# Kernel optimization log

Hardware: AMD Instinct MI355X
Metric: run time of the kernel (lower is better)

## Reference

```python
import jax, jax.numpy as jnp
import numpy as np

S, N, F_IN, F_OUT = 8, 4096, 128, 128


def setup_inputs() -> dict:
    key = jax.random.key(0)
    ks = jax.random.split(key, 7)
    return {
        "theta": jax.random.normal(ks[0], (S,), dtype=jnp.float32),
        "T_slices": jax.random.normal(ks[1], (S, N, N), dtype=jnp.float32),
        "x": jax.random.normal(ks[2], (N, F_IN), dtype=jnp.float32),
        "a": jax.random.uniform(ks[3], (N, N), dtype=jnp.float32),
        "W_fc": jax.random.normal(ks[4], (F_OUT, F_IN), dtype=jnp.float32) * (1.0 / np.sqrt(F_IN)),
        "b_fc": jax.random.normal(ks[5], (F_OUT,), dtype=jnp.float32) * 0.01,
        "prelu_alpha": jnp.full((F_IN,), 0.25, dtype=jnp.float32),
    }


def reference(theta, T_slices, x, a, W_fc, b_fc, prelu_alpha):
    # q = sum_s theta[s] * T_slices[s]  -> [N, N]
    q = jnp.einsum("s,snm->nm", theta, T_slices)
    # mask by adjacency (the torch code then converts to sparse; math is identical)
    q = q * a
    # diffused features: [N, N] @ [N, F_in] -> [N, F_in]
    out = q @ x
    # per-channel PReLU over the feature dim (num_parameters = input_dim)
    out = jnp.where(out >= 0, out, prelu_alpha * out)
    # final linear: out @ W_fc.T + b_fc -> [N, F_out]
    return out @ W_fc.T + b_fc
```

## Files before the change

kernel.cpp:

```cpp
#include <hip/hip_runtime.h>
#include <stdint.h>

constexpr int N  = 4096;
constexpr int F  = 128;
constexpr int S  = 8;
constexpr int BM = 16;
constexpr int BK = 256;
constexpr int NCH = N / BK;
constexpr int NPAIR = NCH * 4;
constexpr int NT = 512;

typedef float f4  __attribute__((ext_vector_type(4)));
typedef short bf16x8 __attribute__((ext_vector_type(8)));
typedef unsigned short us4 __attribute__((ext_vector_type(4)));

__device__ __forceinline__ unsigned short f2bf(float f) {
  union { float f; unsigned int u; } v; v.f = f;
  unsigned int u = v.u + 0x7FFFu + ((v.u >> 16) & 1u);
  return (unsigned short)(u >> 16);
}

__device__ __forceinline__ void bar_sync() {
  asm volatile("s_waitcnt lgkmcnt(0)" ::: "memory");
  __builtin_amdgcn_s_barrier();
  asm volatile("" ::: "memory");
}
__device__ __forceinline__ void vm_wait0() {
  asm volatile("s_waitcnt vmcnt(0)" ::: "memory");
}
__device__ __forceinline__ void vm_wait4() {
  asm volatile("s_waitcnt vmcnt(4)" ::: "memory");
}

__device__ __forceinline__ void gload_lds16(const void* g, void* l) {
  __builtin_amdgcn_global_load_lds(
      (const __attribute__((address_space(1))) void*)g,
      (__attribute__((address_space(3))) void*)l, 16, 0, 0);
}

__global__ __launch_bounds__(256, 2) void ggd_xt(
    const float* __restrict__ x, unsigned short* __restrict__ xT) {
  __shared__ float xl[64][132];
  const int t  = threadIdx.x;
  const int k0 = blockIdx.x * 64;
  {
    const int kr = t >> 2, fs = (t & 3) * 32;
    const float* src = x + (size_t)(k0 + kr) * F + fs;
#pragma unroll
    for (int i = 0; i < 8; ++i)
      *(f4*)&xl[kr][fs + i * 4] = *(const f4*)(src + i * 4);
  }
  __syncthreads();
  {
    const int f = t >> 1, kh = (t & 1) * 32;
    us4 o[8];
#pragma unroll
    for (int i = 0; i < 32; ++i)
      o[i >> 2][i & 3] = f2bf(xl[kh + i][f]);
    unsigned short* dst = xT + (size_t)f * N + k0 + kh;
#pragma unroll
    for (int j = 0; j < 8; ++j)
      *(us4*)(dst + j * 4) = o[j];
  }
}

__global__ __launch_bounds__(NT, 1) void ggd_main(
    const float* __restrict__ theta,
    const float* __restrict__ Ts,
    const unsigned short* __restrict__ xT,
    const float* __restrict__ a,
    const float* __restrict__ W,
    const float* __restrict__ bfc,
    const float* __restrict__ alpha,
    float* __restrict__ out)
{
  __shared__ float rawT[3][2][BM][BK];
  __shared__ unsigned short q_lds[BM][BK];
  __shared__ float p_lds[BM][F];

  const int t    = threadIdx.x;
  const int n0   = blockIdx.x * BM;
  const int wave = t >> 6, lane = t & 63;
  const size_t slice = (size_t)N * N;

  float th[S];
#pragma unroll
  for (int s = 0; s < S; ++s) th[s] = theta[s];

  const int arow = t >> 5;
  const int m0   = t & 31;
  const int rsw  = 2 * (arow & 7);
  const int ms0  = m0 ^ rsw;

  auto stage = [&](int cq, int pq, int slot) {
    const size_t colb = (size_t)cq * BK;
#pragma unroll
    for (int j = 0; j < 4; ++j) {
      const int idx = wave * 4 + j;
      const int sl  = idx >> 4;
      const int row = idx & 15;
      const int s   = 2 * pq + sl;
      const float* src = Ts + (size_t)s * slice + (size_t)(n0 + row) * N +
                         colb + 4 * (lane ^ (2 * (row & 7)));
      gload_lds16(src, &rawT[slot][sl][row][0]);
    }
  };

  f4 av[2];
  auto aload = [&](int c) {
#pragma unroll
    for (int j = 0; j < 2; ++j)
      av[j] = *(const f4*)(a + (size_t)(n0 + arow) * N + c * BK +
                           4 * (m0 + 32 * j));
  };

  f4 acc = (f4)(0.f);

  int cm3 = 0;

  aload(0);
  stage(0, 0, 0);
  stage(0, 1, 1);

  for (int c = 0; c < NCH; ++c) {
    f4 qacc[2] = {(f4)(0.f), (f4)(0.f)};

#pragma unroll
    for (int p = 0; p < 4; ++p) {
      const int P = c * 4 + p;
      if (P == NPAIR - 1) vm_wait0(); else vm_wait4();
      bar_sync();
      if (P + 2 < NPAIR) {
        const int Q  = P + 2;
        const int cq = (p < 2) ? c : c + 1;
        const int pq = (p < 2) ? p + 2 : p - 2;
        stage(cq, pq, (cm3 + p + 2) % 3);
      }
      {
        const int slot = (cm3 + p) % 3;
#pragma unroll
        for (int sl = 0; sl < 2; ++sl) {
          const float* base = &rawT[slot][sl][arow][0];
          const float ths = th[2 * p + sl];
#pragma unroll
          for (int j = 0; j < 2; ++j) {
            f4 tv = *(const f4*)(base + 4 * (ms0 + 32 * j));
#pragma unroll
            for (int e = 0; e < 4; ++e)
              qacc[j][e] = fmaf(ths, tv[e], qacc[j][e]);
          }
        }
      }
    }

#pragma unroll
    for (int j = 0; j < 2; ++j) {
      us4 o;
#pragma unroll
      for (int e = 0; e < 4; ++e) o[e] = f2bf(av[j][e] * qacc[j][e]);
      const int elem = (4 * (m0 + 32 * j)) ^ (8 * (arow & 7));
      *(us4*)&q_lds[arow][elem] = o;
    }
    bar_sync();

    bf16x8 B[8];
    {
      const unsigned short* fp =
          xT + (size_t)(wave * 16 + (lane & 15)) * N + c * BK +
          (lane >> 4) * 8;
#pragma unroll
      for (int k = 0; k < 8; ++k) B[k] = *(const bf16x8*)(fp + k * 32);
    }
    if (c + 1 < NCH) aload(c + 1);
#pragma unroll
    for (int k = 0; k < 8; ++k) {
      const int elem = (k * 32 + (lane >> 4) * 8) ^ ((lane & 7) << 3);
      bf16x8 af = *(const bf16x8*)&q_lds[lane & 15][elem];
      acc = __builtin_amdgcn_mfma_f32_16x16x32_bf16(af, B[k], acc, 0, 0, 0);
    }

    cm3 = (cm3 + 1) % 3;
  }

  {
    const int fo = wave * 16 + (lane & 15);
    const float al = alpha[fo];
#pragma unroll
    for (int r = 0; r < 4; ++r) {
      float v = acc[r];
      v = v >= 0.f ? v : al * v;
      p_lds[(lane >> 4) * 4 + r][fo] = v;
    }
  }
  bar_sync();

  {
    const int r2  = t >> 5;
    const int fo4 = (t & 31) * 4;
    f4 accF = *(const f4*)(bfc + fo4);
#pragma unroll 4
    for (int fi4 = 0; fi4 < F / 4; ++fi4) {
      f4 pv = *(const f4*)&p_lds[r2][fi4 * 4];
#pragma unroll
      for (int e = 0; e < 4; ++e) {
        f4 wv = *(const f4*)(W + (size_t)(fo4 + e) * F + fi4 * 4);
        accF[e] = fmaf(pv[0], wv[0], fmaf(pv[1], wv[1],
                  fmaf(pv[2], wv[2], fmaf(pv[3], wv[3], accF[e]))));
      }
    }
    *(f4*)(out + (size_t)(n0 + r2) * F + fo4) = accF;
  }
}

__global__ __launch_bounds__(256, 1) void ggd_fused_fb(
    const float* __restrict__ theta, const float* __restrict__ Ts,
    const float* __restrict__ x, const float* __restrict__ a,
    const float* __restrict__ W, const float* __restrict__ bfc,
    const float* __restrict__ alpha, float* __restrict__ out) {
  constexpr int BMf = 16, BKf = 64, NCF = N / BKf;
  __shared__ float q_l[2][BMf][BKf];
  __shared__ float p_l[BMf][F];
  const int t  = threadIdx.x;
  const int n0 = blockIdx.x * BMf;
  float th[S];
#pragma unroll
  for (int s = 0; s < S; ++s) th[s] = theta[s];
  const int qr = t >> 4, qk = (t & 15) << 2;
  const size_t rowOff = (size_t)(n0 + qr) * N, sliceSz = (size_t)N * N;
  const int tx = t & 31, ty = t >> 5;
  const int r0 = ty * 2, r1 = r0 + 1;
  f4 acc0 = (f4)(0.f), acc1 = (f4)(0.f);
  f4 tv[S]; f4 avv;
  auto loadc = [&](int c) {
    const size_t off = rowOff + (size_t)c * BKf + qk;
    avv = *(const f4*)(a + off);
#pragma unroll
    for (int s = 0; s < S; ++s)
      tv[s] = *(const f4*)(Ts + (size_t)s * sliceSz + off);
  };
  auto qstore = [&](int buf) {
    f4 qv;
#pragma unroll
    for (int j = 0; j < 4; ++j) {
      float sum = th[0] * tv[0][j];
#pragma unroll
      for (int s = 1; s < S; ++s) sum = fmaf(th[s], tv[s][j], sum);
      qv[j] = avv[j] * sum;
    }
    *(f4*)&q_l[buf][qr][qk] = qv;
  };
  loadc(0); qstore(0);
  for (int c = 0; c < NCF; ++c) {
    const int buf = c & 1;
    if (c + 1 < NCF) loadc(c + 1);
    bar_sync();
    const float* xp = x + (size_t)c * BKf * F + tx * 4;
#pragma unroll 4
    for (int kk4 = 0; kk4 < BKf / 4; ++kk4) {
      f4 q0 = *(const f4*)&q_l[buf][r0][kk4 * 4];
      f4 q1 = *(const f4*)&q_l[buf][r1][kk4 * 4];
#pragma unroll
      for (int j = 0; j < 4; ++j) {
        f4 xv = *(const f4*)(xp + (size_t)(kk4 * 4 + j) * F);
#pragma unroll
        for (int e = 0; e < 4; ++e) {
          acc0[e] = fmaf(q0[j], xv[e], acc0[e]);
          acc1[e] = fmaf(q1[j], xv[e], acc1[e]);
        }
      }
    }
    if (c + 1 < NCF) qstore(buf ^ 1);
  }
  {
    f4 al = *(const f4*)(alpha + tx * 4);
#pragma unroll
    for (int j = 0; j < 4; ++j) {
      acc0[j] = acc0[j] >= 0.f ? acc0[j] : al[j] * acc0[j];
      acc1[j] = acc1[j] >= 0.f ? acc1[j] : al[j] * acc1[j];
    }
  }
  *(f4*)&p_l[r0][tx * 4] = acc0;
  *(f4*)&p_l[r1][tx * 4] = acc1;
  bar_sync();
  const int rr = t >> 4, fo0 = (t & 15) * 8;
  float accF[8];
  {
    f4 b0 = *(const f4*)(bfc + fo0);
    f4 b1 = *(const f4*)(bfc + fo0 + 4);
#pragma unroll
    for (int j = 0; j < 4; ++j) { accF[j] = b0[j]; accF[4 + j] = b1[j]; }
  }
#pragma unroll 8
  for (int fi4 = 0; fi4 < F / 4; ++fi4) {
    f4 p4 = *(const f4*)&p_l[rr][fi4 * 4];
#pragma unroll
    for (int j = 0; j < 8; ++j) {
      f4 w4 = *(const f4*)(W + (size_t)(fo0 + j) * F + fi4 * 4);
      accF[j] = fmaf(p4[0], w4[0], fmaf(p4[1], w4[1],
                fmaf(p4[2], w4[2], fmaf(p4[3], w4[3], accF[j]))));
    }
  }
  f4 o0, o1;
#pragma unroll
  for (int j = 0; j < 4; ++j) { o0[j] = accF[j]; o1[j] = accF[4 + j]; }
  float* op = out + (size_t)(n0 + rr) * F + fo0;
  *(f4*)op       = o0;
  *(f4*)(op + 4) = o1;
}

extern "C" void kernel_launch(void* const* d_in, const int* in_sizes, int n_in,
                              void* d_out, int out_size, void* d_ws, size_t ws_size,
                              hipStream_t stream) {
  const float* theta = (const float*)d_in[0];
  const float* Ts    = (const float*)d_in[1];
  const float* x     = (const float*)d_in[2];
  const float* a     = (const float*)d_in[3];
  const float* W     = (const float*)d_in[4];
  const float* bfc   = (const float*)d_in[5];
  const float* alpha = (const float*)d_in[6];
  float* out = (float*)d_out;

  const size_t xt_bytes = (size_t)N * F * 2;
  if (ws_size >= xt_bytes && d_ws != nullptr) {
    unsigned short* xT = (unsigned short*)d_ws;
    ggd_xt  <<<dim3(N / 64), dim3(256), 0, stream>>>(x, xT);
    ggd_main<<<dim3(N / BM), dim3(NT), 0, stream>>>(
        theta, Ts, xT, a, W, bfc, alpha, out);
  } else {
    ggd_fused_fb<<<dim3(N / 16), dim3(256), 0, stream>>>(
        theta, Ts, x, a, W, bfc, alpha, out);
  }
}
```

Before: 170.9 us.

## Split-K across independent waves with per-wave staging and separate FC kernel

Restructures the main kernel so that each wave independently owns a 16-row block and one quarter of the K range. It stages all 8 T slices for a 32-wide K chunk into private LDS double buffers and builds the bf16 q fragment directly in registers, with no block-wide barriers. Partial results go to a workspace, and a new kernel sums the four partials, then applies PReLU and the final linear layer. This removes barrier synchronisation and the LDS round-trip for q, at the cost of extra global traffic for the partials, an additional kernel launch, and a larger workspace requirement that could fall back to the slow path.

Result: slower. 179.5 us (+5.0%).

```diff
diff --git a/kernel.cpp b/kernel.cpp
--- a/kernel.cpp
+++ b/kernel.cpp
@@ -5,14 +5,16 @@
 constexpr int F  = 128;
 constexpr int S  = 8;
 constexpr int BM = 16;
-constexpr int BK = 256;
-constexpr int NCH = N / BK;
-constexpr int NPAIR = NCH * 4;
-constexpr int NT = 512;
+constexpr int KSPLIT = 4;
+constexpr int KRANGE = N / KSPLIT;
+constexpr int BK = 32;
+constexpr int NCH = KRANGE / BK;
+constexpr int NT = 256;
 
 typedef float f4  __attribute__((ext_vector_type(4)));
 typedef short bf16x8 __attribute__((ext_vector_type(8)));
 typedef unsigned short us4 __attribute__((ext_vector_type(4)));
+typedef unsigned short us8 __attribute__((ext_vector_type(8)));
 
 __device__ __forceinline__ unsigned short f2bf(float f) {
   union { float f; unsigned int u; } v; v.f = f;
@@ -24,12 +26,6 @@
   asm volatile("s_waitcnt lgkmcnt(0)" ::: "memory");
   __builtin_amdgcn_s_barrier();
   asm volatile("" ::: "memory");
-}
-__device__ __forceinline__ void vm_wait0() {
-  asm volatile("s_waitcnt vmcnt(0)" ::: "memory");
-}
-__device__ __forceinline__ void vm_wait4() {
-  asm volatile("s_waitcnt vmcnt(4)" ::: "memory");
 }
 
 __device__ __forceinline__ void gload_lds16(const void* g, void* l) {
@@ -64,152 +60,160 @@
   }
 }
 
-__global__ __launch_bounds__(NT, 1) void ggd_main(
+__global__ __launch_bounds__(NT, 1) void ggd_wave(
     const float* __restrict__ theta,
     const float* __restrict__ Ts,
     const unsigned short* __restrict__ xT,
     const float* __restrict__ a,
+    float* __restrict__ parts)
+{
+  __shared__ float rawT[4][2][S][BM][BK];
+
+  const int t    = threadIdx.x;
+  const int wave = t >> 6, lane = t & 63;
+  const int wid  = blockIdx.x * 4 + wave;
+  const int rb   = wid >> 2;
+  const int ks   = wid & 3;
+  const int n0   = rb * BM;
+  const int k0   = ks * KRANGE;
+  const size_t slice = (size_t)N * N;
+
+  float th[S];
+#pragma unroll
+  for (int s = 0; s < S; ++s) th[s] = theta[s];
+
+  const int r   = lane & 15;
+  const int kb  = 8 * (lane >> 4);
+  const int kb4 = 2 * (lane >> 4);
+  const int rs  = r & 7;
+
+  const int g_row = lane >> 3;
+  const int g_k4  = (lane & 7) ^ g_row;
+
+  auto stage = [&](int c, int buf) {
+    const size_t col = (size_t)(k0 + c * BK) + 4 * g_k4;
+    float* dst0 = &rawT[wave][buf][0][0][0];
+#pragma unroll
+    for (int j = 0; j < 16; ++j) {
+      const int s = j >> 1, h = j & 1;
+      const float* src = Ts + (size_t)s * slice +
+                         (size_t)(n0 + h * 8 + g_row) * N + col;
+      gload_lds16(src, dst0 + (size_t)s * (BM * BK) + h * 8 * BK);
+    }
+  };
+
+  f4 acc[8];
+#pragma unroll
+  for (int i = 0; i < 8; ++i) acc[i] = (f4)(0.f);
+
+  stage(0, 0);
+
+  for (int c = 0; c < NCH; ++c) {
+    const int kc = k0 + c * BK;
+
+    bf16x8 B[8];
+#pragma unroll
+    for (int i = 0; i < 8; ++i)
+      B[i] = *(const bf16x8*)(xT + (size_t)(i * 16 + r) * N + kc + kb);
+    f4 av0 = *(const f4*)(a + (size_t)(n0 + r) * N + kc + kb);
+    f4 av1 = *(const f4*)(a + (size_t)(n0 + r) * N + kc + kb + 4);
+    asm volatile("" ::: "memory");
+
+    if (c + 1 < NCH) {
+      stage(c + 1, (c + 1) & 1);
+      asm volatile("s_waitcnt vmcnt(16)" ::: "memory");
+    } else {
+      asm volatile("s_waitcnt vmcnt(0)" ::: "memory");
+    }
+
+    const float* base = &rawT[wave][c & 1][0][r][0];
+    f4 s0 = (f4)(0.f), s1 = (f4)(0.f);
+#pragma unroll
+    for (int s = 0; s < S; ++s) {
+      const float* bs = base + (size_t)s * (BM * BK);
+      f4 t0 = *(const f4*)(bs + 4 * ((kb4 + 0) ^ rs));
+      f4 t1 = *(const f4*)(bs + 4 * ((kb4 + 1) ^ rs));
+#pragma unroll
+      for (int e = 0; e < 4; ++e) {
+        s0[e] = fmaf(th[s], t0[e], s0[e]);
+        s1[e] = fmaf(th[s], t1[e], s1[e]);
+      }
+    }
+    us8 u;
+#pragma unroll
+    for (int e = 0; e < 4; ++e) {
+      u[e]     = f2bf(av0[e] * s0[e]);
+      u[4 + e] = f2bf(av1[e] * s1[e]);
+    }
+    bf16x8 af = *(bf16x8*)&u;
+
+#pragma unroll
+    for (int i = 0; i < 8; ++i)
+      acc[i] = __builtin_amdgcn_mfma_f32_16x16x32_bf16(af, B[i], acc[i],
+                                                       0, 0, 0);
+  }
+
+  const int crow = n0 + (lane >> 4) * 4;
+#pragma unroll
+  for (int i = 0; i < 8; ++i) {
+    const int fo = i * 16 + r;
+#pragma unroll
+    for (int rr = 0; rr < 4; ++rr)
+      parts[((size_t)ks * N + crow + rr) * F + fo] = acc[i][rr];
+  }
+}
+
+__global__ __launch_bounds__(256, 2) void ggd_fc(
     const float* __restrict__ W,
     const float* __restrict__ bfc,
     const float* __restrict__ alpha,
+    const float* __restrict__ src,
     float* __restrict__ out)
 {
-  __shared__ float rawT[3][2][BM][BK];
-  __shared__ unsigned short q_lds[BM][BK];
-  __shared__ float p_lds[BM][F];
-
-  const int t    = threadIdx.x;
-  const int n0   = blockIdx.x * BM;
-  const int wave = t >> 6, lane = t & 63;
-  const size_t slice = (size_t)N * N;
-
-  float th[S];
-#pragma unroll
-  for (int s = 0; s < S; ++s) th[s] = theta[s];
-
-  const int arow = t >> 5;
-  const int m0   = t & 31;
-  const int rsw  = 2 * (arow & 7);
-  const int ms0  = m0 ^ rsw;
-
-  auto stage = [&](int cq, int pq, int slot) {
-    const size_t colb = (size_t)cq * BK;
+  __shared__ float p_lds[16 * F];
+  const int t  = threadIdx.x;
+  const int n0 = blockIdx.x * 16;
+
+  {
+    const int lr = t >> 4, c8 = (t & 15) * 8;
+    f4 v0 = (f4)(0.f), v1 = (f4)(0.f);
+#pragma unroll
+    for (int ks = 0; ks < KSPLIT; ++ks) {
+      const float* sp = src + ((size_t)ks * N + n0 + lr) * F + c8;
+      v0 += *(const f4*)(sp);
+      v1 += *(const f4*)(sp + 4);
+    }
+    f4 a0 = *(const f4*)(alpha + c8);
+    f4 a1 = *(const f4*)(alpha + c8 + 4);
 #pragma unroll
     for (int j = 0; j < 4; ++j) {
-      const int idx = wave * 4 + j;
-      const int sl  = idx >> 4;
-      const int row = idx & 15;
-      const int s   = 2 * pq + sl;
-      const float* src = Ts + (size_t)s * slice + (size_t)(n0 + row) * N +
-                         colb + 4 * (lane ^ (2 * (row & 7)));
-      gload_lds16(src, &rawT[slot][sl][row][0]);
-    }
-  };
-
-  f4 av[2];
-  auto aload = [&](int c) {
-#pragma unroll
-    for (int j = 0; j < 2; ++j)
-      av[j] = *(const f4*)(a + (size_t)(n0 + arow) * N + c * BK +
-                           4 * (m0 + 32 * j));
-  };
-
-  f4 acc = (f4)(0.f);
-
-  int cm3 = 0;
-
-  aload(0);
-  stage(0, 0, 0);
-  stage(0, 1, 1);
-
-  for (int c = 0; c < NCH; ++c) {
-    f4 qacc[2] = {(f4)(0.f), (f4)(0.f)};
-
-#pragma unroll
-    for (int p = 0; p < 4; ++p) {
-      const int P = c * 4 + p;
-      if (P == NPAIR - 1) vm_wait0(); else vm_wait4();
-      bar_sync();
-      if (P + 2 < NPAIR) {
-        const int Q  = P + 2;
-        const int cq = (p < 2) ? c : c + 1;
-        const int pq = (p < 2) ? p + 2 : p - 2;
-        stage(cq, pq, (cm3 + p + 2) % 3);
-      }
-      {
-        const int slot = (cm3 + p) % 3;
-#pragma unroll
-        for (int sl = 0; sl < 2; ++sl) {
-          const float* base = &rawT[slot][sl][arow][0];
-          const float ths = th[2 * p + sl];
-#pragma unroll
-          for (int j = 0; j < 2; ++j) {
-            f4 tv = *(const f4*)(base + 4 * (ms0 + 32 * j));
-#pragma unroll
-            for (int e = 0; e < 4; ++e)
-              qacc[j][e] = fmaf(ths, tv[e], qacc[j][e]);
-          }
-        }
-      }
-    }
-
-#pragma unroll
-    for (int j = 0; j < 2; ++j) {
-      us4 o;
-#pragma unroll
-      for (int e = 0; e < 4; ++e) o[e] = f2bf(av[j][e] * qacc[j][e]);
-      const int elem = (4 * (m0 + 32 * j)) ^ (8 * (arow & 7));
-      *(us4*)&q_lds[arow][elem] = o;
-    }
-    bar_sync();
-
-    bf16x8 B[8];
-    {
-      const unsigned short* fp =
-          xT + (size_t)(wave * 16 + (lane & 15)) * N + c * BK +
-          (lane >> 4) * 8;
-#pragma unroll
-      for (int k = 0; k < 8; ++k) B[k] = *(const bf16x8*)(fp + k * 32);
-    }
-    if (c + 1 < NCH) aload(c + 1);
-#pragma unroll
-    for (int k = 0; k < 8; ++k) {
-      const int elem = (k * 32 + (lane >> 4) * 8) ^ ((lane & 7) << 3);
-      bf16x8 af = *(const bf16x8*)&q_lds[lane & 15][elem];
-      acc = __builtin_amdgcn_mfma_f32_16x16x32_bf16(af, B[k], acc, 0, 0, 0);
-    }
-
-    cm3 = (cm3 + 1) % 3;
-  }
-
-  {
-    const int fo = wave * 16 + (lane & 15);
-    const float al = alpha[fo];
-#pragma unroll
-    for (int r = 0; r < 4; ++r) {
-      float v = acc[r];
-      v = v >= 0.f ? v : al * v;
-      p_lds[(lane >> 4) * 4 + r][fo] = v;
-    }
-  }
-  bar_sync();
-
-  {
-    const int r2  = t >> 5;
-    const int fo4 = (t & 31) * 4;
-    f4 accF = *(const f4*)(bfc + fo4);
+      v0[j] = v0[j] >= 0.f ? v0[j] : a0[j] * v0[j];
+      v1[j] = v1[j] >= 0.f ? v1[j] : a1[j] * v1[j];
+    }
+    *(f4*)&p_lds[lr * F + c8]     = v0;
+    *(f4*)&p_lds[lr * F + c8 + 4] = v1;
+  }
+  __syncthreads();
+
+  const int r2  = t >> 5;
+  const int fo0 = (t & 31) * 4;
+  f4 accA = *(const f4*)(bfc + fo0);
+  f4 accB = accA;
 #pragma unroll 4
-    for (int fi4 = 0; fi4 < F / 4; ++fi4) {
-      f4 pv = *(const f4*)&p_lds[r2][fi4 * 4];
-#pragma unroll
-      for (int e = 0; e < 4; ++e) {
-        f4 wv = *(const f4*)(W + (size_t)(fo4 + e) * F + fi4 * 4);
-        accF[e] = fmaf(pv[0], wv[0], fmaf(pv[1], wv[1],
-                  fmaf(pv[2], wv[2], fmaf(pv[3], wv[3], accF[e]))));
-      }
-    }
-    *(f4*)(out + (size_t)(n0 + r2) * F + fo4) = accF;
-  }
+  for (int fi4 = 0; fi4 < F / 4; ++fi4) {
+    f4 pA = *(const f4*)&p_lds[r2 * F + fi4 * 4];
+    f4 pB = *(const f4*)&p_lds[(r2 + 8) * F + fi4 * 4];
+#pragma unroll
+    for (int e = 0; e < 4; ++e) {
+      f4 wv = *(const f4*)(W + (size_t)(fo0 + e) * F + fi4 * 4);
+      accA[e] = fmaf(pA[0], wv[0], fmaf(pA[1], wv[1],
+                fmaf(pA[2], wv[2], fmaf(pA[3], wv[3], accA[e]))));
+      accB[e] = fmaf(pB[0], wv[0], fmaf(pB[1], wv[1],
+                fmaf(pB[2], wv[2], fmaf(pB[3], wv[3], accB[e]))));
+    }
+  }
+  *(f4*)(out + (size_t)(n0 + r2) * F + fo0)     = accA;
+  *(f4*)(out + (size_t)(n0 + r2 + 8) * F + fo0) = accB;
 }
 
 __global__ __launch_bounds__(256, 1) void ggd_fused_fb(
@@ -320,12 +324,16 @@
   const float* alpha = (const float*)d_in[6];
   float* out = (float*)d_out;
 
-  const size_t xt_bytes = (size_t)N * F * 2;
-  if (ws_size >= xt_bytes && d_ws != nullptr) {
-    unsigned short* xT = (unsigned short*)d_ws;
+  const size_t part_bytes = (size_t)KSPLIT * N * F * sizeof(float);
+  const size_t xt_bytes   = (size_t)N * F * 2;
+  if (ws_size >= part_bytes + xt_bytes && d_ws != nullptr) {
+    float* parts = (float*)d_ws;
+    unsigned short* xT = (unsigned short*)((char*)d_ws + part_bytes);
     ggd_xt  <<<dim3(N / 64), dim3(256), 0, stream>>>(x, xT);
-    ggd_main<<<dim3(N / BM), dim3(NT), 0, stream>>>(
-        theta, Ts, xT, a, W, bfc, alpha, out);
+    ggd_wave<<<dim3((N / BM) * KSPLIT / 4), dim3(NT), 0, stream>>>(
+        theta, Ts, xT, a, parts);
+    ggd_fc  <<<dim3(N / 16), dim3(256), 0, stream>>>(
+        W, bfc, alpha, parts, out);
   } else {
     ggd_fused_fb<<<dim3(N / 16), dim3(256), 0, stream>>>(
         theta, Ts, x, a, W, bfc, alpha, out);
```

## Split q generation into streaming kernel and separate bf16 MFMA GEMM kernel

Applied to the files above, without the earlier changes.

Replaces the single fused kernel, which staged T slices through LDS per 16-row block, with two kernels. A grid-wide streaming kernel computes theta-weighted sums of the T slices, masks by a, and writes bf16 q with a swizzled layout to workspace. A separate GEMM kernel uses 8-row tiles, triple-buffered async LDS loads of q, and MFMA against bf16 xT, followed by the PReLU and FC epilogue. The aim is to expose more memory-level parallelism for the dominant 512MB T read, at the cost of an extra 32MB q write and read and a larger workspace requirement.

Measured after the change: 216.6 us. +26.8%, slower.

```diff
diff --git a/kernel.cpp b/kernel.cpp
--- a/kernel.cpp
+++ b/kernel.cpp
@@ -4,11 +4,6 @@
 constexpr int N  = 4096;
 constexpr int F  = 128;
 constexpr int S  = 8;
-constexpr int BM = 16;
-constexpr int BK = 256;
-constexpr int NCH = N / BK;
-constexpr int NPAIR = NCH * 4;
-constexpr int NT = 512;
 
 typedef float f4  __attribute__((ext_vector_type(4)));
 typedef short bf16x8 __attribute__((ext_vector_type(8)));
@@ -25,11 +20,11 @@
   __builtin_amdgcn_s_barrier();
   asm volatile("" ::: "memory");
 }
-__device__ __forceinline__ void vm_wait0() {
+__device__ __forceinline__ void vm_drain() {
   asm volatile("s_waitcnt vmcnt(0)" ::: "memory");
 }
-__device__ __forceinline__ void vm_wait4() {
-  asm volatile("s_waitcnt vmcnt(4)" ::: "memory");
+__device__ __forceinline__ void vm_wait1() {
+  asm volatile("s_waitcnt vmcnt(1)" ::: "memory");
 }
 
 __device__ __forceinline__ void gload_lds16(const void* g, void* l) {
@@ -64,151 +59,154 @@
   }
 }
 
-__global__ __launch_bounds__(NT, 1) void ggd_main(
+constexpr int QF4 = N / 4;
+constexpr int TOT = N * QF4;
+constexpr int POS = 8;
+constexpr int QG_BLOCKS = TOT / (256 * POS);
+constexpr int QG_STRIDE = 256 * QG_BLOCKS;
+
+__global__ __launch_bounds__(256, 4) void ggd_qgen(
     const float* __restrict__ theta,
     const float* __restrict__ Ts,
+    const float* __restrict__ a,
+    unsigned short* __restrict__ q)
+{
+  float th[S];
+#pragma unroll
+  for (int s = 0; s < S; ++s) th[s] = theta[s];
+
+  const int tid = blockIdx.x * 256 + threadIdx.x;
+  const f4* tf4 = (const f4*)Ts;
+  const f4* af4 = (const f4*)a;
+  us4* qs = (us4*)q;
+
+  f4 acc[POS];
+#pragma unroll
+  for (int s = 0; s < S; ++s) {
+    f4 tv[POS];
+#pragma unroll
+    for (int ii = 0; ii < POS; ++ii)
+      tv[ii] = tf4[(size_t)s * TOT + tid + ii * QG_STRIDE];
+    if (s == 0) {
+#pragma unroll
+      for (int ii = 0; ii < POS; ++ii)
+#pragma unroll
+        for (int e = 0; e < 4; ++e)
+          acc[ii][e] = th[0] * tv[ii][e];
+    } else {
+#pragma unroll
+      for (int ii = 0; ii < POS; ++ii)
+#pragma unroll
+        for (int e = 0; e < 4; ++e)
+          acc[ii][e] = fmaf(th[s], tv[ii][e], acc[ii][e]);
+    }
+  }
+#pragma unroll
+  for (int ii = 0; ii < POS; ++ii) {
+    const int idx = tid + ii * QG_STRIDE;
+    f4 av = af4[idx];
+    us4 o;
+#pragma unroll
+    for (int e = 0; e < 4; ++e) o[e] = f2bf(av[e] * acc[ii][e]);
+    const int r  = idx >> 10;
+    const int k4 = idx & (QF4 - 1);
+    qs[(size_t)r * QF4 + (k4 ^ ((r & 7) << 1))] = o;
+  }
+}
+
+constexpr int GBM = 8;
+constexpr int GBK = 256;
+constexpr int GNC = N / GBK;
+
+__global__ __launch_bounds__(256, 2) void ggd_gemm(
+    const unsigned short* __restrict__ q,
     const unsigned short* __restrict__ xT,
-    const float* __restrict__ a,
     const float* __restrict__ W,
     const float* __restrict__ bfc,
     const float* __restrict__ alpha,
     float* __restrict__ out)
 {
-  __shared__ float rawT[3][2][BM][BK];
-  __shared__ unsigned short q_lds[BM][BK];
-  __shared__ float p_lds[BM][F];
-
-  const int t    = threadIdx.x;
-  const int n0   = blockIdx.x * BM;
-  const int wave = t >> 6, lane = t & 63;
-  const size_t slice = (size_t)N * N;
-
-  float th[S];
-#pragma unroll
-  for (int s = 0; s < S; ++s) th[s] = theta[s];
-
-  const int arow = t >> 5;
-  const int m0   = t & 31;
-  const int rsw  = 2 * (arow & 7);
-  const int ms0  = m0 ^ rsw;
-
-  auto stage = [&](int cq, int pq, int slot) {
-    const size_t colb = (size_t)cq * BK;
-#pragma unroll
-    for (int j = 0; j < 4; ++j) {
-      const int idx = wave * 4 + j;
-      const int sl  = idx >> 4;
-      const int row = idx & 15;
-      const int s   = 2 * pq + sl;
-      const float* src = Ts + (size_t)s * slice + (size_t)(n0 + row) * N +
-                         colb + 4 * (lane ^ (2 * (row & 7)));
-      gload_lds16(src, &rawT[slot][sl][row][0]);
-    }
+  __shared__ unsigned short qt[3][GBM][GBK];
+  __shared__ float p_lds[GBM][F];
+
+  const int t = threadIdx.x, wave = t >> 6, lane = t & 63;
+  const int n0 = blockIdx.x * GBM;
+
+  auto stage = [&](int c, int buf) {
+    const int row = wave * 2 + (lane >> 5);
+    const unsigned short* src =
+        q + (size_t)(n0 + row) * N + c * GBK + (lane & 31) * 8;
+    gload_lds16(src, &qt[buf][wave * 2][0]);
   };
 
-  f4 av[2];
-  auto aload = [&](int c) {
-#pragma unroll
-    for (int j = 0; j < 2; ++j)
-      av[j] = *(const f4*)(a + (size_t)(n0 + arow) * N + c * BK +
-                           4 * (m0 + 32 * j));
-  };
-
-  f4 acc = (f4)(0.f);
-
-  int cm3 = 0;
-
-  aload(0);
-  stage(0, 0, 0);
-  stage(0, 1, 1);
-
-  for (int c = 0; c < NCH; ++c) {
-    f4 qacc[2] = {(f4)(0.f), (f4)(0.f)};
-
-#pragma unroll
-    for (int p = 0; p < 4; ++p) {
-      const int P = c * 4 + p;
-      if (P == NPAIR - 1) vm_wait0(); else vm_wait4();
-      bar_sync();
-      if (P + 2 < NPAIR) {
-        const int Q  = P + 2;
-        const int cq = (p < 2) ? c : c + 1;
-        const int pq = (p < 2) ? p + 2 : p - 2;
-        stage(cq, pq, (cm3 + p + 2) % 3);
+  f4 acc[2];
+#pragma unroll
+  for (int i = 0; i < 2; ++i) acc[i] = (f4)(0.f);
+
+  const int rr  = lane & 7;
+  const int rsw = rr << 3;
+
+  stage(0, 0);
+  stage(1, 1);
+
+  for (int c = 0; c < GNC; ++c) {
+    const int buf = c % 3;
+    if (c + 2 < GNC) stage(c + 2, (c + 2) % 3);
+
+    bf16x8 B[16];
+#pragma unroll
+    for (int i = 0; i < 2; ++i) {
+      const unsigned short* fp =
+          xT + (size_t)((wave * 2 + i) * 16 + (lane & 15)) * N + c * GBK +
+          (lane >> 4) * 8;
+#pragma unroll
+      for (int h = 0; h < 8; ++h)
+        B[i * 8 + h] = *(const bf16x8*)(fp + h * 32);
+    }
+
+    if (c == GNC - 1) vm_drain(); else vm_wait1();
+    bar_sync();
+
+#pragma unroll
+    for (int h = 0; h < 8; ++h) {
+      const int elem = (h * 32 + (lane >> 4) * 8) ^ rsw;
+      bf16x8 af = *(const bf16x8*)&qt[buf][rr][elem];
+      acc[0] = __builtin_amdgcn_mfma_f32_16x16x32_bf16(af, B[h],     acc[0], 0, 0, 0);
+      acc[1] = __builtin_amdgcn_mfma_f32_16x16x32_bf16(af, B[8 + h], acc[1], 0, 0, 0);
+    }
+    bar_sync();
+  }
+
+  if (lane < 32) {
+#pragma unroll
+    for (int i = 0; i < 2; ++i) {
+      const int fo = (wave * 2 + i) * 16 + (lane & 15);
+      const float al = alpha[fo];
+#pragma unroll
+      for (int r = 0; r < 4; ++r) {
+        float v = acc[i][r];
+        v = v >= 0.f ? v : al * v;
+        p_lds[(lane >> 4) * 4 + r][fo] = v;
       }
-      {
-        const int slot = (cm3 + p) % 3;
-#pragma unroll
-        for (int sl = 0; sl < 2; ++sl) {
-          const float* base = &rawT[slot][sl][arow][0];
-          const float ths = th[2 * p + sl];
-#pragma unroll
-          for (int j = 0; j < 2; ++j) {
-            f4 tv = *(const f4*)(base + 4 * (ms0 + 32 * j));
-#pragma unroll
-            for (int e = 0; e < 4; ++e)
-              qacc[j][e] = fmaf(ths, tv[e], qacc[j][e]);
-          }
-        }
-      }
-    }
-
-#pragma unroll
-    for (int j = 0; j < 2; ++j) {
-      us4 o;
-#pragma unroll
-      for (int e = 0; e < 4; ++e) o[e] = f2bf(av[j][e] * qacc[j][e]);
-      const int elem = (4 * (m0 + 32 * j)) ^ (8 * (arow & 7));
-      *(us4*)&q_lds[arow][elem] = o;
-    }
-    bar_sync();
-
-    bf16x8 B[8];
-    {
-      const unsigned short* fp =
-          xT + (size_t)(wave * 16 + (lane & 15)) * N + c * BK +
-          (lane >> 4) * 8;
-#pragma unroll
-      for (int k = 0; k < 8; ++k) B[k] = *(const bf16x8*)(fp + k * 32);
-    }
-    if (c + 1 < NCH) aload(c + 1);
-#pragma unroll
-    for (int k = 0; k < 8; ++k) {
-      const int elem = (k * 32 + (lane >> 4) * 8) ^ ((lane & 7) << 3);
-      bf16x8 af = *(const bf16x8*)&q_lds[lane & 15][elem];
-      acc = __builtin_amdgcn_mfma_f32_16x16x32_bf16(af, B[k], acc, 0, 0, 0);
-    }
-
-    cm3 = (cm3 + 1) % 3;
-  }
-
-  {
-    const int fo = wave * 16 + (lane & 15);
-    const float al = alpha[fo];
-#pragma unroll
-    for (int r = 0; r < 4; ++r) {
-      float v = acc[r];
-      v = v >= 0.f ? v : al * v;
-      p_lds[(lane >> 4) * 4 + r][fo] = v;
     }
   }
   bar_sync();
 
   {
     const int r2  = t >> 5;
-    const int fo4 = (t & 31) * 4;
-    f4 accF = *(const f4*)(bfc + fo4);
+    const int fo0 = (t & 31) * 4;
+    f4 accF = *(const f4*)(bfc + fo0);
 #pragma unroll 4
     for (int fi4 = 0; fi4 < F / 4; ++fi4) {
       f4 pv = *(const f4*)&p_lds[r2][fi4 * 4];
 #pragma unroll
       for (int e = 0; e < 4; ++e) {
-        f4 wv = *(const f4*)(W + (size_t)(fo4 + e) * F + fi4 * 4);
+        f4 wv = *(const f4*)(W + (size_t)(fo0 + e) * F + fi4 * 4);
         accF[e] = fmaf(pv[0], wv[0], fmaf(pv[1], wv[1],
                   fmaf(pv[2], wv[2], fmaf(pv[3], wv[3], accF[e]))));
       }
     }
-    *(f4*)(out + (size_t)(n0 + r2) * F + fo4) = accF;
+    *(f4*)(out + (size_t)(n0 + r2) * F + fo0) = accF;
   }
 }
 
@@ -320,12 +318,15 @@
   const float* alpha = (const float*)d_in[6];
   float* out = (float*)d_out;
 
+  const size_t q_bytes  = (size_t)N * N * 2;
   const size_t xt_bytes = (size_t)N * F * 2;
-  if (ws_size >= xt_bytes && d_ws != nullptr) {
-    unsigned short* xT = (unsigned short*)d_ws;
-    ggd_xt  <<<dim3(N / 64), dim3(256), 0, stream>>>(x, xT);
-    ggd_main<<<dim3(N / BM), dim3(NT), 0, stream>>>(
-        theta, Ts, xT, a, W, bfc, alpha, out);
+  if (ws_size >= q_bytes + xt_bytes && d_ws != nullptr) {
+    unsigned short* qbuf = (unsigned short*)d_ws;
+    unsigned short* xT   = (unsigned short*)((char*)d_ws + q_bytes);
+    ggd_xt  <<<dim3(N / 64),     dim3(256), 0, stream>>>(x, xT);
+    ggd_qgen<<<dim3(QG_BLOCKS),  dim3(256), 0, stream>>>(theta, Ts, a, qbuf);
+    ggd_gemm<<<dim3(N / GBM),    dim3(256), 0, stream>>>(qbuf, xT, W, bfc,
+                                                         alpha, out);
   } else {
     ggd_fused_fb<<<dim3(N / 16), dim3(256), 0, stream>>>(
         theta, Ts, x, a, W, bfc, alpha, out);
```
